# Performance work log

Measured on AMD Instinct MI355X. Metric: run time of the kernel, lower is better.

## Reference

```python
import jax, jax.numpy as jnp
import numpy as np

NUM_Q_HEADS = 32
NUM_KV_HEADS = 8
HEAD_DIM = 128
HIDDEN = 4096
EPS = 1e-6
ROPE_THETA = 1e6


def _rmsnorm(t, w):
    # per-head RMSNorm over last dim (head_dim), as in skip_rmsnorm with residual=None
    var = jnp.mean(t * t, axis=-1, keepdims=True)
    return t * jax.lax.rsqrt(var + EPS) * w


def _rotate_half(t):
    h = t.shape[-1] // 2
    return jnp.concatenate([-t[..., h:], t[..., :h]], axis=-1)


def setup_inputs() -> dict:
    key = jax.random.key(0)
    ks = jax.random.split(key, 4)
    B, S = 2, 1024
    x = jax.random.normal(ks[0], (B, S, HIDDEN), jnp.float32)
    q_proj_w = jax.random.normal(ks[1], (HIDDEN, NUM_Q_HEADS * HEAD_DIM), jnp.float32) * 0.02
    kv_proj_w = jax.random.normal(ks[2], (HIDDEN, 2 * NUM_KV_HEADS * HEAD_DIM), jnp.float32) * 0.02
    o_proj_w = jax.random.normal(ks[3], (NUM_Q_HEADS * HEAD_DIM, HIDDEN), jnp.float32) * 0.02
    q_norm_w = jnp.ones((HEAD_DIM,), jnp.float32)
    k_norm_w = jnp.ones((HEAD_DIM,), jnp.float32)
    # real rotate-half RoPE tables, shape [S, head_dim]
    inv_freq = 1.0 / (ROPE_THETA ** (jnp.arange(0, HEAD_DIM, 2, dtype=jnp.float32) / HEAD_DIM))
    freqs = jnp.arange(S, dtype=jnp.float32)[:, None] * inv_freq[None, :]  # [S, hd/2]
    emb = jnp.concatenate([freqs, freqs], axis=-1)  # [S, hd]
    cos, sin = jnp.cos(emb), jnp.sin(emb)
    kv_buffer = jnp.zeros((16384, 2 * NUM_KV_HEADS, HEAD_DIM), jnp.float32)
    cur_select_index = jnp.arange(B * S, dtype=jnp.int32)
    return {"x": x, "q_proj_w": q_proj_w, "kv_proj_w": kv_proj_w, "o_proj_w": o_proj_w,
            "q_norm_w": q_norm_w, "k_norm_w": k_norm_w, "cos": cos, "sin": sin,
            "kv_buffer": kv_buffer, "cur_select_index": cur_select_index}


def reference(x, q_proj_w, kv_proj_w, o_proj_w, q_norm_w, k_norm_w, cos, sin, kv_buffer, cur_select_index):
    B, S, _ = x.shape
    T = B * S
    xf = x.reshape(T, HIDDEN)
    # projections (weights stored as [in, out])
    xq = (xf @ q_proj_w).reshape(T, NUM_Q_HEADS, HEAD_DIM)
    xkv = xf @ kv_proj_w
    xk = xkv[:, : NUM_KV_HEADS * HEAD_DIM].reshape(T, NUM_KV_HEADS, HEAD_DIM)
    xv = xkv[:, NUM_KV_HEADS * HEAD_DIM:].reshape(T, NUM_KV_HEADS, HEAD_DIM)
    # per-head RMSNorm (Qwen3 q/k norm)
    xq = _rmsnorm(xq, q_norm_w)
    xk = _rmsnorm(xk, k_norm_w)
    # RoPE (cos/sin are [S, hd], tiled over batch, broadcast over heads)
    cos_t = jnp.tile(cos, (B, 1))[:, None, :]  # [T,1,hd]
    sin_t = jnp.tile(sin, (B, 1))[:, None, :]
    xq = xq * cos_t + _rotate_half(xq) * sin_t
    xk = xk * cos_t + _rotate_half(xk) * sin_t
    # paged KV-cache scatter update (update_kv_buffer)
    combined_kv = jnp.concatenate([xk, xv], axis=1)  # [T, 2*Hk, hd]
    buf = kv_buffer.at[cur_select_index].set(combined_kv)
    # ragged causal flash attention (equal per-request lengths here), GQA expand
    rep = NUM_Q_HEADS // NUM_KV_HEADS
    q = xq.reshape(B, S, NUM_Q_HEADS, HEAD_DIM)
    k = jnp.repeat(xk.reshape(B, S, NUM_KV_HEADS, HEAD_DIM), rep, axis=2)
    v = jnp.repeat(xv.reshape(B, S, NUM_KV_HEADS, HEAD_DIM), rep, axis=2)
    scale = HEAD_DIM ** -0.5
    scores = jnp.einsum('bqhd,bkhd->bhqk', q, k) * scale  # [B,H,S,S]
    causal = jnp.tril(jnp.ones((S, S), bool))
    scores = jnp.where(causal[None, None], scores, jnp.float32(-1e30))
    p = jax.nn.softmax(scores, axis=-1)
    attn = jnp.einsum('bhqk,bkhd->bqhd', p, v).reshape(B, S, NUM_Q_HEADS * HEAD_DIM)
    out = attn @ o_proj_w  # [B,S,hidden]
    return out, buf
```

## Files before the change

### kernel.cpp

```cpp
#include <hip/hip_runtime.h>

typedef float fx4 __attribute__((ext_vector_type(4)));
typedef short s16x4 __attribute__((ext_vector_type(4)));
typedef short s16x8 __attribute__((ext_vector_type(8)));
typedef __bf16 bf16x8 __attribute__((ext_vector_type(8)));

__device__ __forceinline__ short f2bf(float f) {
  unsigned u = __builtin_bit_cast(unsigned, f);
  u += 0x7fffu + ((u >> 16) & 1u);
  return (short)(u >> 16);
}
__device__ __forceinline__ float b2f(short s) {
  unsigned u = ((unsigned)(unsigned short)s) << 16;
  return __builtin_bit_cast(float, u);
}

__device__ __forceinline__ bf16x8 ld8(const short* p) {
  s16x8 v = *(const s16x8*)p;
  return __builtin_bit_cast(bf16x8, v);
}

__device__ __forceinline__ void gld16(const void* g, void* l) {
  __builtin_amdgcn_global_load_lds(
      (const __attribute__((address_space(1))) unsigned*)g,
      (__attribute__((address_space(3))) unsigned*)l, 16, 0, 0);
}

template<int N> __device__ __forceinline__ void wait_vmcnt() {
  if constexpr (N == 0)      asm volatile("s_waitcnt vmcnt(0)" ::: "memory");
  else if constexpr (N == 4) asm volatile("s_waitcnt vmcnt(4)" ::: "memory");
  else if constexpr (N == 6) asm volatile("s_waitcnt vmcnt(6)" ::: "memory");
  __builtin_amdgcn_sched_barrier(0);
}

__device__ __forceinline__ void barrier_pin() {
  __builtin_amdgcn_s_barrier();
  __builtin_amdgcn_sched_barrier(0);
}

__global__ __launch_bounds__(256) void cvt_k(const float* __restrict__ in,
                                             short* __restrict__ out) {
  int i = (blockIdx.x * 256 + threadIdx.x) * 8;
  fx4 a = *(const fx4*)(in + i);
  fx4 b = *(const fx4*)(in + i + 4);
  s16x8 w;
  w[0] = f2bf(a[0]); w[1] = f2bf(a[1]); w[2] = f2bf(a[2]); w[3] = f2bf(a[3]);
  w[4] = f2bf(b[0]); w[5] = f2bf(b[1]); w[6] = f2bf(b[2]); w[7] = f2bf(b[3]);
  *(s16x8*)(out + i) = w;
}

__global__ __launch_bounds__(256) void tr_k(const float* __restrict__ in,
    short* __restrict__ out, int K, int N) {
  __shared__ short T[64][72];
  const int ktiles = K >> 6;
  const int tk0 = (blockIdx.x % ktiles) << 6;
  const int tn0 = (blockIdx.x / ktiles) << 6;
  const int tid = threadIdx.x;
  #pragma unroll
  for (int i = 0; i < 4; ++i) {
    int idx = i * 256 + tid;
    int k = idx >> 4, n4 = (idx & 15) << 2;
    fx4 v = *(const fx4*)(in + (size_t)(tk0 + k) * N + tn0 + n4);
    #pragma unroll
    for (int j = 0; j < 4; ++j) T[n4 + j][k] = f2bf(v[j]);
  }
  __syncthreads();
  #pragma unroll
  for (int i = 0; i < 2; ++i) {
    int idx = i * 256 + tid;
    int n = idx >> 3, k8 = (idx & 7) << 3;
    *(s16x8*)(out + (size_t)(tn0 + n) * K + tk0 + k8) = *(const s16x8*)&T[n][k8];
  }
}

__global__ __launch_bounds__(256) void vtr_k(const short* __restrict__ vbp,
                                             short* __restrict__ vbt) {
  __shared__ short T[64][72];
  const int tile = blockIdx.x & 31;
  const int tt = tile & 15, dt = tile >> 4;
  const int bk = blockIdx.x >> 5;
  const int b = bk >> 3, kvh = bk & 7;
  const int t0 = tt << 6, d0 = dt << 6;
  const int tid = threadIdx.x;
  #pragma unroll
  for (int i = 0; i < 2; ++i) {
    int idx = i * 256 + tid;
    int r = idx >> 3, c8 = (idx & 7) << 3;
    s16x8 v = *(const s16x8*)(vbp + (size_t)(b * 1024 + t0 + r) * 1024 + kvh * 128 + d0 + c8);
    #pragma unroll
    for (int j = 0; j < 8; ++j) T[c8 + j][r] = v[j];
  }
  __syncthreads();
  #pragma unroll
  for (int i = 0; i < 2; ++i) {
    int idx = i * 256 + tid;
    int r = idx >> 3, c8 = (idx & 7) << 3;
    *(s16x8*)(vbt + ((size_t)(b * 8 + kvh) * 128 + d0 + r) * 1024 + t0 + c8) =
        *(const s16x8*)&T[r][c8];
  }
}

template<int BF16OUT>
__global__ __launch_bounds__(512) void gemm8(const short* __restrict__ A,
    const short* __restrict__ Bt, void* __restrict__ Cp, int N, int K,
    const fx4* __restrict__ csrc, fx4* __restrict__ cdst, int gemmBlocks,
    size_t nvec) {
  const int tid = threadIdx.x;
  if ((int)blockIdx.x >= gemmBlocks) {
    size_t stride = (size_t)(gridDim.x - gemmBlocks) * 512;
    for (size_t i = (size_t)((int)blockIdx.x - gemmBlocks) * 512 + tid;
         i < nvec; i += stride)
      cdst[i] = csrc[i];
    return;
  }
  __shared__ short As[2][2][128 * 64];
  __shared__ short Bs[2][2][128 * 64];
  const int tiles_n = N >> 8;
  const int tm = blockIdx.x / tiles_n, tn = blockIdx.x % tiles_n;
  const int lane = tid & 63, wv = tid >> 6;
  const int wm = (wv >> 2) << 6;
  const int wn = (wv & 3) << 5;
  const int r0 = tm << 8, c0 = tn << 8;
  const int lrow = lane & 15, lg = lane >> 4;

  auto stageA = [&](int t, int hh) {
    int k0 = t << 6, s = t & 1;
    #pragma unroll
    for (int i = 0; i < 2; ++i) {
      int c = i * 512 + tid;
      int row = c >> 3, ch = c & 7;
      gld16(A + (size_t)(r0 + hh * 128 + row) * K + k0 + ((ch ^ (row & 7)) << 3),
            &As[s][hh][(i * 512 + wv * 64) * 8]);
    }
  };
  auto stageB = [&](int t, int hh) {
    int k0 = t << 6, s = t & 1;
    #pragma unroll
    for (int i = 0; i < 2; ++i) {
      int c = i * 512 + tid;
      int row = c >> 3, ch = c & 7;
      gld16(Bt + (size_t)(c0 + hh * 128 + row) * K + k0 + ((ch ^ (row & 7)) << 3),
            &Bs[s][hh][(i * 512 + wv * 64) * 8]);
    }
  };

  fx4 acc[2][2][4][2] = {};
  bf16x8 a[4][2], b[2][2];

  auto ldA = [&](int s, int hh) {
    #pragma unroll
    for (int mf = 0; mf < 4; ++mf) {
      int lr = wm + mf * 16 + lrow;
      #pragma unroll
      for (int ks = 0; ks < 2; ++ks)
        a[mf][ks] = ld8(&As[s][hh][lr * 64 + ((((ks << 2) + lg) ^ (lr & 7)) << 3)]);
    }
  };
  auto ldB = [&](int s, int hh) {
    #pragma unroll
    for (int nf = 0; nf < 2; ++nf) {
      int lr = wn + nf * 16 + lrow;
      #pragma unroll
      for (int ks = 0; ks < 2; ++ks)
        b[nf][ks] = ld8(&Bs[s][hh][lr * 64 + ((((ks << 2) + lg) ^ (lr & 7)) << 3)]);
    }
  };

  const int nt = K >> 6;
  stageA(0, 0); stageA(0, 1); stageB(0, 0); stageB(0, 1);
  stageA(1, 0); stageB(1, 1);

  for (int t = 0; t < nt; ++t) {
    const int s = t & 1;
    if (t + 1 < nt) wait_vmcnt<4>(); else wait_vmcnt<0>();
    barrier_pin();
    ldA(s, 0); ldB(s, 0);
    if (t + 1 < nt) stageA(t + 1, 1);
    __builtin_amdgcn_s_setprio(1);
    #pragma unroll
    for (int ks = 0; ks < 2; ++ks)
      #pragma unroll
      for (int mf = 0; mf < 4; ++mf)
        #pragma unroll
        for (int nf = 0; nf < 2; ++nf)
          acc[0][0][mf][nf] = __builtin_amdgcn_mfma_f32_16x16x32_bf16(
              a[mf][ks], b[nf][ks], acc[0][0][mf][nf], 0, 0, 0);
    __builtin_amdgcn_s_setprio(0);
    barrier_pin();
    ldB(s, 1);
    if (t + 1 < nt) stageB(t + 1, 0);
    __builtin_amdgcn_s_setprio(1);
    #pragma unroll
    for (int ks = 0; ks < 2; ++ks)
      #pragma unroll
      for (int mf = 0; mf < 4; ++mf)
        #pragma unroll
        for (int nf = 0; nf < 2; ++nf)
          acc[0][1][mf][nf] = __builtin_amdgcn_mfma_f32_16x16x32_bf16(
              a[mf][ks], b[nf][ks], acc[0][1][mf][nf], 0, 0, 0);
    __builtin_amdgcn_s_setprio(0);
    barrier_pin();
    ldA(s, 1);
    if (t + 2 < nt) stageA(t + 2, 0);
    __builtin_amdgcn_s_setprio(1);
    #pragma unroll
    for (int ks = 0; ks < 2; ++ks)
      #pragma unroll
      for (int mf = 0; mf < 4; ++mf)
        #pragma unroll
        for (int nf = 0; nf < 2; ++nf)
          acc[1][1][mf][nf] = __builtin_amdgcn_mfma_f32_16x16x32_bf16(
              a[mf][ks], b[nf][ks], acc[1][1][mf][nf], 0, 0, 0);
    __builtin_amdgcn_s_setprio(0);
    barrier_pin();
    ldB(s, 0);
    if (t + 2 < nt) stageB(t + 2, 1);
    __builtin_amdgcn_s_setprio(1);
    #pragma unroll
    for (int ks = 0; ks < 2; ++ks)
      #pragma unroll
      for (int mf = 0; mf < 4; ++mf)
        #pragma unroll
        for (int nf = 0; nf < 2; ++nf)
          acc[1][0][mf][nf] = __builtin_amdgcn_mfma_f32_16x16x32_bf16(
              a[mf][ks], b[nf][ks], acc[1][0][mf][nf], 0, 0, 0);
    __builtin_amdgcn_s_setprio(0);
    barrier_pin();
  }
  const int g4 = lg << 2;
  #pragma unroll
  for (int mq = 0; mq < 2; ++mq)
    #pragma unroll
    for (int nq = 0; nq < 2; ++nq)
      #pragma unroll
      for (int mf = 0; mf < 4; ++mf)
        #pragma unroll
        for (int nf = 0; nf < 2; ++nf)
          #pragma unroll
          for (int j = 0; j < 4; ++j) {
            int row = r0 + mq * 128 + wm + mf * 16 + g4 + j;
            int col = c0 + nq * 128 + wn + nf * 16 + lrow;
            if (BF16OUT)
              ((short*)Cp)[(size_t)row * N + col] = f2bf(acc[mq][nq][mf][nf][j]);
            else
              ((float*)Cp)[(size_t)row * N + col] = acc[mq][nq][mf][nf][j];
          }
}

__global__ __launch_bounds__(512) void gemm4(const short* __restrict__ A,
    const short* __restrict__ Bt, float* __restrict__ Cp, int N, int K) {
  __shared__ short As[3][2][128 * 64];
  __shared__ short Bs[3][128 * 64];
  const int tiles_n = N >> 7;
  const int tm = blockIdx.x / tiles_n, tn = blockIdx.x % tiles_n;
  const int tid = threadIdx.x;
  const int lane = tid & 63, wv = tid >> 6;
  const int wm = (wv >> 2) << 6;
  const int wn = (wv & 3) << 5;
  const int r0 = tm << 8, c0 = tn << 7;
  const int lrow = lane & 15, lg = lane >> 4;

  auto stageA = [&](int t, int hh) {
    int k0 = t << 6, s = t % 3;
    #pragma unroll
    for (int i = 0; i < 2; ++i) {
      int c = i * 512 + tid;
      int row = c >> 3, ch = c & 7;
      gld16(A + (size_t)(r0 + hh * 128 + row) * K + k0 + ((ch ^ (row & 7)) << 3),
            &As[s][hh][(i * 512 + wv * 64) * 8]);
    }
  };
  auto stageB = [&](int t) {
    int k0 = t << 6, s = t % 3;
    #pragma unroll
    for (int i = 0; i < 2; ++i) {
      int c = i * 512 + tid;
      int row = c >> 3, ch = c & 7;
      gld16(Bt + (size_t)(c0 + row) * K + k0 + ((ch ^ (row & 7)) << 3),
            &Bs[s][(i * 512 + wv * 64) * 8]);
    }
  };

  fx4 acc[2][4][2] = {};
  bf16x8 a[4][2], b[2][2];

  auto ldA = [&](int s, int hh) {
    #pragma unroll
    for (int mf = 0; mf < 4; ++mf) {
      int lr = wm + mf * 16 + lrow;
      #pragma unroll
      for (int ks = 0; ks < 2; ++ks)
        a[mf][ks] = ld8(&As[s][hh][lr * 64 + ((((ks << 2) + lg) ^ (lr & 7)) << 3)]);
    }
  };
  auto ldB = [&](int s) {
    #pragma unroll
    for (int nf = 0; nf < 2; ++nf) {
      int lr = wn + nf * 16 + lrow;
      #pragma unroll
      for (int ks = 0; ks < 2; ++ks)
        b[nf][ks] = ld8(&Bs[s][lr * 64 + ((((ks << 2) + lg) ^ (lr & 7)) << 3)]);
    }
  };

  const int nt = K >> 6;
  stageA(0, 0); stageA(0, 1); stageB(0);
  stageA(1, 0); stageA(1, 1); stageB(1);

  for (int t = 0; t < nt; ++t) {
    const int s = t % 3;
    if (t + 1 < nt) wait_vmcnt<6>(); else wait_vmcnt<0>();
    barrier_pin();
    ldA(s, 0); ldB(s);
    if (t + 2 < nt) stageA(t + 2, 0);
    __builtin_amdgcn_s_setprio(1);
    #pragma unroll
    for (int ks = 0; ks < 2; ++ks)
      #pragma unroll
      for (int mf = 0; mf < 4; ++mf)
        #pragma unroll
        for (int nf = 0; nf < 2; ++nf)
          acc[0][mf][nf] = __builtin_amdgcn_mfma_f32_16x16x32_bf16(
              a[mf][ks], b[nf][ks], acc[0][mf][nf], 0, 0, 0);
    __builtin_amdgcn_s_setprio(0);
    barrier_pin();
    ldA(s, 1);
    if (t + 2 < nt) { stageA(t + 2, 1); stageB(t + 2); }
    __builtin_amdgcn_s_setprio(1);
    #pragma unroll
    for (int ks = 0; ks < 2; ++ks)
      #pragma unroll
      for (int mf = 0; mf < 4; ++mf)
        #pragma unroll
        for (int nf = 0; nf < 2; ++nf)
          acc[1][mf][nf] = __builtin_amdgcn_mfma_f32_16x16x32_bf16(
              a[mf][ks], b[nf][ks], acc[1][mf][nf], 0, 0, 0);
    __builtin_amdgcn_s_setprio(0);
    barrier_pin();
  }
  const int g4 = lg << 2;
  #pragma unroll
  for (int mh = 0; mh < 2; ++mh)
    #pragma unroll
    for (int mf = 0; mf < 4; ++mf)
      #pragma unroll
      for (int nf = 0; nf < 2; ++nf)
        #pragma unroll
        for (int j = 0; j < 4; ++j) {
          int row = r0 + mh * 128 + wm + mf * 16 + g4 + j;
          int col = c0 + wn + nf * 16 + lrow;
          Cp[(size_t)row * N + col] = acc[mh][mf][nf][j];
        }
}

__global__ __launch_bounds__(256) void nr_k(const short* __restrict__ xqkv,
    const float* __restrict__ qnw, const float* __restrict__ knw,
    const float* __restrict__ cosb, const float* __restrict__ sinb,
    const int* __restrict__ idx,
    short* __restrict__ qb, short* __restrict__ kbp, short* __restrict__ vbp,
    float* __restrict__ bufo) {
  int rid = blockIdx.x * 4 + (threadIdx.x >> 6);
  int l = threadIdx.x & 63;
  int type, t, h;
  if (rid < 65536)      { type = 0; t = rid >> 5; h = rid & 31; }
  else if (rid < 81920) { type = 1; int r = rid - 65536; t = r >> 3; h = r & 7; }
  else                  { type = 2; int r = rid - 81920; t = r >> 3; h = r & 7; }
  int s = t & 1023;
  const short* src = xqkv + (size_t)t * 6144 +
                     ((type == 0) ? h * 128 : (type == 1) ? 4096 + h * 128
                                                          : 5120 + h * 128);
  float e0 = b2f(src[l]), e1 = b2f(src[l + 64]);
  float out0, out1;
  if (type < 2) {
    float ss = e0 * e0 + e1 * e1;
    #pragma unroll
    for (int off = 1; off < 64; off <<= 1) ss += __shfl_xor(ss, off);
    float r = rsqrtf(ss * (1.0f / 128.0f) + 1e-6f);
    const float* nw = (type == 0) ? qnw : knw;
    float n0 = e0 * r * nw[l], n1 = e1 * r * nw[l + 64];
    float c0 = cosb[s * 128 + l], c1 = cosb[s * 128 + 64 + l];
    float s0 = sinb[s * 128 + l], s1 = sinb[s * 128 + 64 + l];
    out0 = n0 * c0 - n1 * s0;
    out1 = n1 * c1 + n0 * s1;
  } else { out0 = e0; out1 = e1; }
  if (type == 0) {
    short* d = qb + (size_t)t * 4096 + h * 128;
    d[l] = f2bf(out0); d[l + 64] = f2bf(out1);
  } else {
    int br = idx[t];
    float* bd = bufo + (size_t)br * 2048 + (type == 1 ? 0 : 1024) + h * 128;
    bd[l] = out0; bd[l + 64] = out1;
    short* d = (type == 1) ? kbp + (size_t)t * 1024 + h * 128
                           : vbp + (size_t)t * 1024 + h * 128;
    d[l] = f2bf(out0); d[l + 64] = f2bf(out1);
  }
}

#define KLD 136
#define PLD 72

__global__ __launch_bounds__(512) void attn_k(const short* __restrict__ qb,
    const short* __restrict__ kbp, const short* __restrict__ vbt,
    short* __restrict__ ob) {
  __shared__ short Ks[64 * KLD];
  __shared__ short Vs[128 * 64];
  __shared__ short Ps[8][16 * PLD];
  const int bid = blockIdx.x;
  const int p = 7 - (bid & 7), h = (bid >> 3) & 31, b = bid >> 8;
  const int kvh = h >> 2;
  const int tid = threadIdx.x, lane = tid & 63, w = tid >> 6;
  const int lrow = lane & 15, lg = lane >> 4, lk = lg << 3;
  const int q0 = p << 7;
  const int ktmax = 2 * p + 1;
  const float SC2 = 0.088388347648318447f * 1.4426950408889634f;

  bf16x8 qf[4];
  {
    const short* qp = qb + ((size_t)(b * 1024 + q0 + w * 16 + lrow) * 32 + h) * 128 + lk;
    #pragma unroll
    for (int kb4 = 0; kb4 < 4; ++kb4) qf[kb4] = ld8(qp + kb4 * 32);
  }

  const short* vt_base = vbt + (size_t)(b * 8 + kvh) * 128 * 1024;

  const int sd8 = (tid & 15) << 3;
  s16x8 kreg[2], vreg[2];
  auto ldkv = [&](int kv0) {
    #pragma unroll
    for (int it = 0; it < 2; ++it) {
      int r = (it << 5) + (tid >> 4);
      kreg[it] = *(const s16x8*)(kbp + ((size_t)(b * 1024 + kv0 + r) * 8 + kvh) * 128 + sd8);
      int d = (it << 6) + (tid >> 3);
      vreg[it] = *(const s16x8*)(vt_base + (size_t)d * 1024 + kv0 + ((tid & 7) << 3));
    }
  };
  auto wrkv = [&]() {
    #pragma unroll
    for (int it = 0; it < 2; ++it) {
      int r = (it << 5) + (tid >> 4);
      *(s16x8*)&Ks[r * KLD + sd8] = kreg[it];
      int d = (it << 6) + (tid >> 3);
      *(s16x8*)&Vs[d * 64 + (((tid & 7) ^ (d & 7)) << 3)] = vreg[it];
    }
  };

  float m[4], lsum[4];
  fx4 acc[8] = {};
  #pragma unroll
  for (int j = 0; j < 4; ++j) { m[j] = -3.0e38f; lsum[j] = 0.f; }

  ldkv(0);
  wrkv();
  __syncthreads();

  for (int kt = 0; kt <= ktmax; ++kt) {
    const int kv0 = kt << 6;
    if (kt < ktmax) ldkv((kt + 1) << 6);
    fx4 sf[4];
    #pragma unroll
    for (int nc = 0; nc < 4; ++nc) {
      fx4 z = {0.f, 0.f, 0.f, 0.f};
      sf[nc] = z;
      #pragma unroll
      for (int kb4 = 0; kb4 < 4; ++kb4) {
        bf16x8 kf = ld8(&Ks[(nc * 16 + lrow) * KLD + kb4 * 32 + lk]);
        sf[nc] = __builtin_amdgcn_mfma_f32_16x16x32_bf16(qf[kb4], kf, sf[nc], 0, 0, 0);
      }
    }
    if (kt >= ktmax - 1) {
      #pragma unroll
      for (int nc = 0; nc < 4; ++nc)
        #pragma unroll
        for (int j = 0; j < 4; ++j) {
          int qr = q0 + w * 16 + (lg << 2) + j;
          int kc = kv0 + nc * 16 + lrow;
          if (kc > qr) sf[nc][j] = -3.0e38f;
        }
    }
    float pm[4];
    #pragma unroll
    for (int j = 0; j < 4; ++j) pm[j] = -3.0e38f;
    #pragma unroll
    for (int nc = 0; nc < 4; ++nc)
      #pragma unroll
      for (int j = 0; j < 4; ++j) pm[j] = fmaxf(pm[j], sf[nc][j]);
    #pragma unroll
    for (int j = 0; j < 4; ++j) {
      pm[j] = fmaxf(pm[j], __shfl_xor(pm[j], 1));
      pm[j] = fmaxf(pm[j], __shfl_xor(pm[j], 2));
      pm[j] = fmaxf(pm[j], __shfl_xor(pm[j], 4));
      pm[j] = fmaxf(pm[j], __shfl_xor(pm[j], 8));
    }
    float alpha[4], rs[4];
    #pragma unroll
    for (int j = 0; j < 4; ++j) {
      float mn = fmaxf(m[j], pm[j]);
      alpha[j] = exp2f((m[j] - mn) * SC2);
      m[j] = mn;
      rs[j] = 0.f;
    }
    #pragma unroll
    for (int nc = 0; nc < 4; ++nc)
      #pragma unroll
      for (int j = 0; j < 4; ++j) {
        float pv = exp2f((sf[nc][j] - m[j]) * SC2);
        rs[j] += pv;
        Ps[w][((lg << 2) + j) * PLD + nc * 16 + lrow] = f2bf(pv);
      }
    #pragma unroll
    for (int j = 0; j < 4; ++j) {
      rs[j] += __shfl_xor(rs[j], 1);
      rs[j] += __shfl_xor(rs[j], 2);
      rs[j] += __shfl_xor(rs[j], 4);
      rs[j] += __shfl_xor(rs[j], 8);
      lsum[j] = lsum[j] * alpha[j] + rs[j];
    }
    #pragma unroll
    for (int dg = 0; dg < 8; ++dg)
      #pragma unroll
      for (int j = 0; j < 4; ++j) acc[dg][j] *= alpha[j];
    #pragma unroll
    for (int kb2 = 0; kb2 < 2; ++kb2) {
      bf16x8 pf = ld8(&Ps[w][lrow * PLD + kb2 * 32 + lk]);
      #pragma unroll
      for (int dg = 0; dg < 8; ++dg) {
        int d = dg * 16 + lrow;
        int tch = (kb2 << 2) + lg;
        bf16x8 vf = ld8(&Vs[d * 64 + ((tch ^ (d & 7)) << 3)]);
        acc[dg] = __builtin_amdgcn_mfma_f32_16x16x32_bf16(pf, vf, acc[dg], 0, 0, 0);
      }
    }
    __syncthreads();
    if (kt < ktmax) {
      wrkv();
      __syncthreads();
    }
  }
  #pragma unroll
  for (int j = 0; j < 4; ++j) {
    float rl = 1.0f / lsum[j];
    int t = b * 1024 + q0 + w * 16 + (lg << 2) + j;
    short* op = ob + ((size_t)t * 32 + h) * 128;
    #pragma unroll
    for (int dg = 0; dg < 8; ++dg)
      op[dg * 16 + lrow] = f2bf(acc[dg][j] * rl);
  }
}

extern "C" void kernel_launch(void* const* d_in, const int* in_sizes, int n_in,
                              void* d_out, int out_size, void* d_ws, size_t ws_size,
                              hipStream_t stream) {
  (void)in_sizes; (void)n_in; (void)out_size; (void)ws_size;
  const float* x    = (const float*)d_in[0];
  const float* qw   = (const float*)d_in[1];
  const float* kvw  = (const float*)d_in[2];
  const float* ow   = (const float*)d_in[3];
  const float* qnw  = (const float*)d_in[4];
  const float* knw  = (const float*)d_in[5];
  const float* cosb = (const float*)d_in[6];
  const float* sinb = (const float*)d_in[7];
  const float* kvbf = (const float*)d_in[8];
  const int*   idx  = (const int*)d_in[9];

  float* outp = (float*)d_out;
  float* bufp = outp + (size_t)2048 * 4096;

  char* ws = (char*)d_ws;
  short* xqkv = (short*)ws;
  short* qb   = (short*)(ws + (size_t)2048 * 6144 * 4);
  short* kbp  = (short*)((char*)qb + (size_t)2048 * 4096 * 2);
  short* vbp  = (short*)((char*)kbp + (size_t)2048 * 1024 * 2);
  short* attnb = (short*)(ws + (size_t)2048 * 6144 * 2);
  short* owt   = (short*)((char*)qb + (size_t)2048 * 4096 * 2 + (size_t)2048 * 2048 * 2 * 2);
  short* vbt   = owt;

  short* xb    = (short*)bufp;
  short* wqkvt = (short*)(bufp + (size_t)2048 * 2048);

  cvt_k<<<dim3(4096), dim3(256), 0, stream>>>(x, xb);
  tr_k<<<dim3(64 * 64), dim3(256), 0, stream>>>(qw, wqkvt, 4096, 4096);
  tr_k<<<dim3(64 * 32), dim3(256), 0, stream>>>(kvw, wqkvt + (size_t)4096 * 4096, 4096, 2048);
  {
    const fx4* csrc = (const fx4*)(kvbf + (size_t)8192 * 2048);
    fx4* cdst = (fx4*)(bufp + (size_t)8192 * 2048);
    size_t nvec = (size_t)8192 * 2048 / 4;
    gemm8<1><<<dim3(256), dim3(512), 0, stream>>>(xb, wqkvt, (void*)xqkv, 6144, 4096,
                                                  csrc, cdst, 192, nvec);
  }
  hipMemcpyAsync(bufp + (size_t)2048 * 2048, kvbf + (size_t)2048 * 2048,
                 (size_t)6144 * 2048 * 4, hipMemcpyDeviceToDevice, stream);
  nr_k<<<dim3(98304 / 4), dim3(256), 0, stream>>>(xqkv, qnw, knw, cosb, sinb, idx,
                                                  qb, kbp, vbp, bufp);
  vtr_k<<<dim3(512), dim3(256), 0, stream>>>(vbp, vbt);
  attn_k<<<dim3(2 * 32 * 8), dim3(512), 0, stream>>>(qb, kbp, vbt, attnb);
  tr_k<<<dim3(64 * 64), dim3(256), 0, stream>>>(ow, owt, 4096, 4096);
  gemm4<<<dim3(8 * 32), dim3(512), 0, stream>>>(attnb, owt, outp, 4096, 4096);
}
```

Baseline: 364.1 us.

## Split-K the output GEMM with 256x256 tiles and fold the KV copy into attention

The output projection GEMM now uses 256x256 tiles with a 2-way split-K. Chunk 0 writes fp32 directly, chunk 1 writes bf16 partials, and a small reduction kernel adds them. The tail copy of the KV buffer moves from a hipMemcpyAsync into 64 extra blocks of the attention kernel, so it overlaps with attention compute. The bf16 partial adds rounding error, and the split-K costs an extra reduction pass plus extra memory traffic.

```diff
diff --git a/kernel.cpp b/kernel.cpp
--- a/kernel.cpp
+++ b/kernel.cpp
@@ -247,21 +247,24 @@
           }
 }
 
-__global__ __launch_bounds__(512) void gemm4(const short* __restrict__ A,
-    const short* __restrict__ Bt, float* __restrict__ Cp, int N, int K) {
-  __shared__ short As[3][2][128 * 64];
-  __shared__ short Bs[3][128 * 64];
-  const int tiles_n = N >> 7;
-  const int tm = blockIdx.x / tiles_n, tn = blockIdx.x % tiles_n;
+__global__ __launch_bounds__(512) void gemm8sk(const short* __restrict__ A,
+    const short* __restrict__ Bt, float* __restrict__ Cp,
+    short* __restrict__ pK, int N, int K) {
+  __shared__ short As[2][2][128 * 64];
+  __shared__ short Bs[2][2][128 * 64];
+  const int tiles_n = N >> 8;
+  const int tile = blockIdx.x & 127, chunk = blockIdx.x >> 7;
+  const int tm = tile / tiles_n, tn = tile % tiles_n;
+  const int kOff = chunk << 11;
   const int tid = threadIdx.x;
   const int lane = tid & 63, wv = tid >> 6;
   const int wm = (wv >> 2) << 6;
   const int wn = (wv & 3) << 5;
-  const int r0 = tm << 8, c0 = tn << 7;
+  const int r0 = tm << 8, c0 = tn << 8;
   const int lrow = lane & 15, lg = lane >> 4;
 
   auto stageA = [&](int t, int hh) {
-    int k0 = t << 6, s = t % 3;
+    int k0 = kOff + (t << 6), s = t & 1;
     #pragma unroll
     for (int i = 0; i < 2; ++i) {
       int c = i * 512 + tid;
@@ -270,18 +273,18 @@
             &As[s][hh][(i * 512 + wv * 64) * 8]);
     }
   };
-  auto stageB = [&](int t) {
-    int k0 = t << 6, s = t % 3;
+  auto stageB = [&](int t, int hh) {
+    int k0 = kOff + (t << 6), s = t & 1;
     #pragma unroll
     for (int i = 0; i < 2; ++i) {
       int c = i * 512 + tid;
       int row = c >> 3, ch = c & 7;
-      gld16(Bt + (size_t)(c0 + row) * K + k0 + ((ch ^ (row & 7)) << 3),
-            &Bs[s][(i * 512 + wv * 64) * 8]);
-    }
-  };
-
-  fx4 acc[2][4][2] = {};
+      gld16(Bt + (size_t)(c0 + hh * 128 + row) * K + k0 + ((ch ^ (row & 7)) << 3),
+            &Bs[s][hh][(i * 512 + wv * 64) * 8]);
+    }
+  };
+
+  fx4 acc[2][2][4][2] = {};
   bf16x8 a[4][2], b[2][2];
 
   auto ldA = [&](int s, int hh) {
@@ -293,25 +296,51 @@
         a[mf][ks] = ld8(&As[s][hh][lr * 64 + ((((ks << 2) + lg) ^ (lr & 7)) << 3)]);
     }
   };
-  auto ldB = [&](int s) {
+  auto ldB = [&](int s, int hh) {
     #pragma unroll
     for (int nf = 0; nf < 2; ++nf) {
       int lr = wn + nf * 16 + lrow;
       #pragma unroll
       for (int ks = 0; ks < 2; ++ks)
-        b[nf][ks] = ld8(&Bs[s][lr * 64 + ((((ks << 2) + lg) ^ (lr & 7)) << 3)]);
-    }
-  };
-
-  const int nt = K >> 6;
-  stageA(0, 0); stageA(0, 1); stageB(0);
-  stageA(1, 0); stageA(1, 1); stageB(1);
+        b[nf][ks] = ld8(&Bs[s][hh][lr * 64 + ((((ks << 2) + lg) ^ (lr & 7)) << 3)]);
+    }
+  };
+
+  const int nt = 32;
+  stageA(0, 0); stageA(0, 1); stageB(0, 0); stageB(0, 1);
+  stageA(1, 0); stageB(1, 1);
 
   for (int t = 0; t < nt; ++t) {
-    const int s = t % 3;
-    if (t + 1 < nt) wait_vmcnt<6>(); else wait_vmcnt<0>();
-    barrier_pin();
-    ldA(s, 0); ldB(s);
+    const int s = t & 1;
+    if (t + 1 < nt) wait_vmcnt<4>(); else wait_vmcnt<0>();
+    barrier_pin();
+    ldA(s, 0); ldB(s, 0);
+    if (t + 1 < nt) stageA(t + 1, 1);
+    __builtin_amdgcn_s_setprio(1);
+    #pragma unroll
+    for (int ks = 0; ks < 2; ++ks)
+      #pragma unroll
+      for (int mf = 0; mf < 4; ++mf)
+        #pragma unroll
+        for (int nf = 0; nf < 2; ++nf)
+          acc[0][0][mf][nf] = __builtin_amdgcn_mfma_f32_16x16x32_bf16(
+              a[mf][ks], b[nf][ks], acc[0][0][mf][nf], 0, 0, 0);
+    __builtin_amdgcn_s_setprio(0);
+    barrier_pin();
+    ldB(s, 1);
+    if (t + 1 < nt) stageB(t + 1, 0);
+    __builtin_amdgcn_s_setprio(1);
+    #pragma unroll
+    for (int ks = 0; ks < 2; ++ks)
+      #pragma unroll
+      for (int mf = 0; mf < 4; ++mf)
+        #pragma unroll
+        for (int nf = 0; nf < 2; ++nf)
+          acc[0][1][mf][nf] = __builtin_amdgcn_mfma_f32_16x16x32_bf16(
+              a[mf][ks], b[nf][ks], acc[0][1][mf][nf], 0, 0, 0);
+    __builtin_amdgcn_s_setprio(0);
+    barrier_pin();
+    ldA(s, 1);
     if (t + 2 < nt) stageA(t + 2, 0);
     __builtin_amdgcn_s_setprio(1);
     #pragma unroll
@@ -320,37 +349,51 @@
       for (int mf = 0; mf < 4; ++mf)
         #pragma unroll
         for (int nf = 0; nf < 2; ++nf)
-          acc[0][mf][nf] = __builtin_amdgcn_mfma_f32_16x16x32_bf16(
-              a[mf][ks], b[nf][ks], acc[0][mf][nf], 0, 0, 0);
-    __builtin_amdgcn_s_setprio(0);
-    barrier_pin();
-    ldA(s, 1);
-    if (t + 2 < nt) { stageA(t + 2, 1); stageB(t + 2); }
-    __builtin_amdgcn_s_setprio(1);
-    #pragma unroll
-    for (int ks = 0; ks < 2; ++ks)
-      #pragma unroll
-      for (int mf = 0; mf < 4; ++mf)
-        #pragma unroll
-        for (int nf = 0; nf < 2; ++nf)
-          acc[1][mf][nf] = __builtin_amdgcn_mfma_f32_16x16x32_bf16(
-              a[mf][ks], b[nf][ks], acc[1][mf][nf], 0, 0, 0);
+          acc[1][1][mf][nf] = __builtin_amdgcn_mfma_f32_16x16x32_bf16(
+              a[mf][ks], b[nf][ks], acc[1][1][mf][nf], 0, 0, 0);
+    __builtin_amdgcn_s_setprio(0);
+    barrier_pin();
+    ldB(s, 0);
+    if (t + 2 < nt) stageB(t + 2, 1);
+    __builtin_amdgcn_s_setprio(1);
+    #pragma unroll
+    for (int ks = 0; ks < 2; ++ks)
+      #pragma unroll
+      for (int mf = 0; mf < 4; ++mf)
+        #pragma unroll
+        for (int nf = 0; nf < 2; ++nf)
+          acc[1][0][mf][nf] = __builtin_amdgcn_mfma_f32_16x16x32_bf16(
+              a[mf][ks], b[nf][ks], acc[1][0][mf][nf], 0, 0, 0);
     __builtin_amdgcn_s_setprio(0);
     barrier_pin();
   }
   const int g4 = lg << 2;
   #pragma unroll
-  for (int mh = 0; mh < 2; ++mh)
-    #pragma unroll
-    for (int mf = 0; mf < 4; ++mf)
-      #pragma unroll
-      for (int nf = 0; nf < 2; ++nf)
-        #pragma unroll
-        for (int j = 0; j < 4; ++j) {
-          int row = r0 + mh * 128 + wm + mf * 16 + g4 + j;
-          int col = c0 + wn + nf * 16 + lrow;
-          Cp[(size_t)row * N + col] = acc[mh][mf][nf][j];
-        }
+  for (int mq = 0; mq < 2; ++mq)
+    #pragma unroll
+    for (int nq = 0; nq < 2; ++nq)
+      #pragma unroll
+      for (int mf = 0; mf < 4; ++mf)
+        #pragma unroll
+        for (int nf = 0; nf < 2; ++nf)
+          #pragma unroll
+          for (int j = 0; j < 4; ++j) {
+            int row = r0 + mq * 128 + wm + mf * 16 + g4 + j;
+            int col = c0 + nq * 128 + wn + nf * 16 + lrow;
+            if (chunk == 0)
+              Cp[(size_t)row * N + col] = acc[mq][nq][mf][nf][j];
+            else
+              pK[(size_t)row * N + col] = f2bf(acc[mq][nq][mf][nf][j]);
+          }
+}
+
+__global__ __launch_bounds__(256) void red_k(float* __restrict__ outp,
+                                             const short* __restrict__ pK) {
+  size_t i = ((size_t)blockIdx.x * 256 + threadIdx.x) * 4;
+  fx4 o = *(fx4*)(outp + i);
+  s16x4 p = *(const s16x4*)(pK + i);
+  o[0] += b2f(p[0]); o[1] += b2f(p[1]); o[2] += b2f(p[2]); o[3] += b2f(p[3]);
+  *(fx4*)(outp + i) = o;
 }
 
 __global__ __launch_bounds__(256) void nr_k(const short* __restrict__ xqkv,
@@ -398,17 +441,26 @@
 
 #define KLD 136
 #define PLD 72
+#define CPB 64
 
 __global__ __launch_bounds__(512) void attn_k(const short* __restrict__ qb,
     const short* __restrict__ kbp, const short* __restrict__ vbt,
-    short* __restrict__ ob) {
+    short* __restrict__ ob, const fx4* __restrict__ csrc,
+    fx4* __restrict__ cdst, size_t nvec) {
   __shared__ short Ks[64 * KLD];
   __shared__ short Vs[128 * 64];
   __shared__ short Ps[8][16 * PLD];
-  const int bid = blockIdx.x;
+  const int tid = threadIdx.x;
+  if ((int)blockIdx.x < CPB) {
+    size_t stride = (size_t)CPB * 512;
+    for (size_t i = (size_t)blockIdx.x * 512 + tid; i < nvec; i += stride)
+      cdst[i] = csrc[i];
+    return;
+  }
+  const int bid = blockIdx.x - CPB;
   const int p = 7 - (bid & 7), h = (bid >> 3) & 31, b = bid >> 8;
   const int kvh = h >> 2;
-  const int tid = threadIdx.x, lane = tid & 63, w = tid >> 6;
+  const int lane = tid & 63, w = tid >> 6;
   const int lrow = lane & 15, lg = lane >> 4, lk = lg << 3;
   const int q0 = p << 7;
   const int ktmax = 2 * p + 1;
@@ -573,6 +625,7 @@
   short* attnb = (short*)(ws + (size_t)2048 * 6144 * 2);
   short* owt   = (short*)((char*)qb + (size_t)2048 * 4096 * 2 + (size_t)2048 * 2048 * 2 * 2);
   short* vbt   = owt;
+  short* pK    = xqkv;
 
   short* xb    = (short*)bufp;
   short* wqkvt = (short*)(bufp + (size_t)2048 * 2048);
@@ -587,12 +640,17 @@
     gemm8<1><<<dim3(256), dim3(512), 0, stream>>>(xb, wqkvt, (void*)xqkv, 6144, 4096,
                                                   csrc, cdst, 192, nvec);
   }
-  hipMemcpyAsync(bufp + (size_t)2048 * 2048, kvbf + (size_t)2048 * 2048,
-                 (size_t)6144 * 2048 * 4, hipMemcpyDeviceToDevice, stream);
   nr_k<<<dim3(98304 / 4), dim3(256), 0, stream>>>(xqkv, qnw, knw, cosb, sinb, idx,
                                                   qb, kbp, vbp, bufp);
   vtr_k<<<dim3(512), dim3(256), 0, stream>>>(vbp, vbt);
-  attn_k<<<dim3(2 * 32 * 8), dim3(512), 0, stream>>>(qb, kbp, vbt, attnb);
+  {
+    const fx4* csrc = (const fx4*)(kvbf + (size_t)2048 * 2048);
+    fx4* cdst = (fx4*)(bufp + (size_t)2048 * 2048);
+    size_t nvec = (size_t)6144 * 2048 / 4;
+    attn_k<<<dim3(2 * 32 * 8 + CPB), dim3(512), 0, stream>>>(qb, kbp, vbt, attnb,
+                                                             csrc, cdst, nvec);
+  }
   tr_k<<<dim3(64 * 64), dim3(256), 0, stream>>>(ow, owt, 4096, 4096);
-  gemm4<<<dim3(8 * 32), dim3(512), 0, stream>>>(attnb, owt, outp, 4096, 4096);
-}
+  gemm8sk<<<dim3(256), dim3(512), 0, stream>>>(attnb, owt, outp, pK, 4096, 4096);
+  red_k<<<dim3(8192), dim3(256), 0, stream>>>(outp, pK);
+}
```

After: 396.6 us. 1.09x slower.

## Merge prologue kernels and overlap o_proj weight transpose with attention

Applied to the files above, without the earlier changes.

Folds the x conversion and both QKV weight transposes into one prologue launch. The o_proj weight transpose moves into 64 extra blocks of the attention kernel so it runs alongside attention instead of as a separate kernel. The KV-buffer copy moves to the end of the stream, and owt now reuses the bufp scratch region that the copy later overwrites. This removes launch gaps and tail idle time, at the cost of tying up 64 CUs with transpose work during attention and depending on the copy ordering for correctness of the buffer region.

```diff
diff --git a/kernel.cpp b/kernel.cpp
--- a/kernel.cpp
+++ b/kernel.cpp
@@ -38,24 +38,27 @@
   __builtin_amdgcn_sched_barrier(0);
 }
 
-__global__ __launch_bounds__(256) void cvt_k(const float* __restrict__ in,
-                                             short* __restrict__ out) {
-  int i = (blockIdx.x * 256 + threadIdx.x) * 8;
-  fx4 a = *(const fx4*)(in + i);
-  fx4 b = *(const fx4*)(in + i + 4);
-  s16x8 w;
-  w[0] = f2bf(a[0]); w[1] = f2bf(a[1]); w[2] = f2bf(a[2]); w[3] = f2bf(a[3]);
-  w[4] = f2bf(b[0]); w[5] = f2bf(b[1]); w[6] = f2bf(b[2]); w[7] = f2bf(b[3]);
-  *(s16x8*)(out + i) = w;
-}
-
-__global__ __launch_bounds__(256) void tr_k(const float* __restrict__ in,
-    short* __restrict__ out, int K, int N) {
+__global__ __launch_bounds__(256) void pro_k(const float* __restrict__ x,
+    short* __restrict__ xb, const float* __restrict__ qw,
+    const float* __restrict__ kvw, short* __restrict__ wqkvt) {
   __shared__ short T[64][72];
-  const int ktiles = K >> 6;
-  const int tk0 = (blockIdx.x % ktiles) << 6;
-  const int tn0 = (blockIdx.x / ktiles) << 6;
   const int tid = threadIdx.x;
+  const int blk = blockIdx.x;
+  if (blk < 4096) {
+    int i = (blk * 256 + tid) * 8;
+    fx4 a = *(const fx4*)(x + i);
+    fx4 b = *(const fx4*)(x + i + 4);
+    s16x8 w;
+    w[0] = f2bf(a[0]); w[1] = f2bf(a[1]); w[2] = f2bf(a[2]); w[3] = f2bf(a[3]);
+    w[4] = f2bf(b[0]); w[5] = f2bf(b[1]); w[6] = f2bf(b[2]); w[7] = f2bf(b[3]);
+    *(s16x8*)(xb + i) = w;
+    return;
+  }
+  const float* in; short* out; int N, t;
+  if (blk < 8192) { in = qw;  out = wqkvt;                          N = 4096; t = blk - 4096; }
+  else            { in = kvw; out = wqkvt + (size_t)4096 * 4096;    N = 2048; t = blk - 8192; }
+  const int tk0 = (t & 63) << 6;
+  const int tn0 = (t >> 6) << 6;
   #pragma unroll
   for (int i = 0; i < 4; ++i) {
     int idx = i * 256 + tid;
@@ -69,7 +72,7 @@
   for (int i = 0; i < 2; ++i) {
     int idx = i * 256 + tid;
     int n = idx >> 3, k8 = (idx & 7) << 3;
-    *(s16x8*)(out + (size_t)(tn0 + n) * K + tk0 + k8) = *(const s16x8*)&T[n][k8];
+    *(s16x8*)(out + (size_t)(tn0 + n) * 4096 + tk0 + k8) = *(const s16x8*)&T[n][k8];
   }
 }
 
@@ -398,17 +401,42 @@
 
 #define KLD 136
 #define PLD 72
+#define TRB 64
 
 __global__ __launch_bounds__(512) void attn_k(const short* __restrict__ qb,
     const short* __restrict__ kbp, const short* __restrict__ vbt,
-    short* __restrict__ ob) {
+    short* __restrict__ ob, const float* __restrict__ ow,
+    short* __restrict__ owt) {
   __shared__ short Ks[64 * KLD];
   __shared__ short Vs[128 * 64];
   __shared__ short Ps[8][16 * PLD];
-  const int bid = blockIdx.x;
+  const int tid = threadIdx.x;
+  if ((int)blockIdx.x < TRB) {
+    short (*T)[72] = (short(*)[72])Ks;
+    for (int t = (int)blockIdx.x; t < 4096; t += TRB) {
+      const int tk0 = (t & 63) << 6;
+      const int tn0 = (t >> 6) << 6;
+      #pragma unroll
+      for (int i = 0; i < 2; ++i) {
+        int idx = i * 512 + tid;
+        int k = idx >> 4, n4 = (idx & 15) << 2;
+        fx4 v = *(const fx4*)(ow + (size_t)(tk0 + k) * 4096 + tn0 + n4);
+        #pragma unroll
+        for (int j = 0; j < 4; ++j) T[n4 + j][k] = f2bf(v[j]);
+      }
+      __syncthreads();
+      {
+        int n = tid >> 3, k8 = (tid & 7) << 3;
+        *(s16x8*)(owt + (size_t)(tn0 + n) * 4096 + tk0 + k8) = *(const s16x8*)&T[n][k8];
+      }
+      __syncthreads();
+    }
+    return;
+  }
+  const int bid = blockIdx.x - TRB;
   const int p = 7 - (bid & 7), h = (bid >> 3) & 31, b = bid >> 8;
   const int kvh = h >> 2;
-  const int tid = threadIdx.x, lane = tid & 63, w = tid >> 6;
+  const int lane = tid & 63, w = tid >> 6;
   const int lrow = lane & 15, lg = lane >> 4, lk = lg << 3;
   const int q0 = p << 7;
   const int ktmax = 2 * p + 1;
@@ -567,19 +595,17 @@
 
   char* ws = (char*)d_ws;
   short* xqkv = (short*)ws;
+  short* attnb = (short*)(ws + (size_t)2048 * 6144 * 2);
   short* qb   = (short*)(ws + (size_t)2048 * 6144 * 4);
   short* kbp  = (short*)((char*)qb + (size_t)2048 * 4096 * 2);
   short* vbp  = (short*)((char*)kbp + (size_t)2048 * 1024 * 2);
-  short* attnb = (short*)(ws + (size_t)2048 * 6144 * 2);
-  short* owt   = (short*)((char*)qb + (size_t)2048 * 4096 * 2 + (size_t)2048 * 2048 * 2 * 2);
-  short* vbt   = owt;
+  short* vbt  = (short*)((char*)vbp + (size_t)2048 * 1024 * 2);
 
   short* xb    = (short*)bufp;
   short* wqkvt = (short*)(bufp + (size_t)2048 * 2048);
-
-  cvt_k<<<dim3(4096), dim3(256), 0, stream>>>(x, xb);
-  tr_k<<<dim3(64 * 64), dim3(256), 0, stream>>>(qw, wqkvt, 4096, 4096);
-  tr_k<<<dim3(64 * 32), dim3(256), 0, stream>>>(kvw, wqkvt + (size_t)4096 * 4096, 4096, 2048);
+  short* owt   = (short*)(bufp + (size_t)2048 * 2048);
+
+  pro_k<<<dim3(10240), dim3(256), 0, stream>>>(x, xb, qw, kvw, wqkvt);
   {
     const fx4* csrc = (const fx4*)(kvbf + (size_t)8192 * 2048);
     fx4* cdst = (fx4*)(bufp + (size_t)8192 * 2048);
@@ -587,12 +613,11 @@
     gemm8<1><<<dim3(256), dim3(512), 0, stream>>>(xb, wqkvt, (void*)xqkv, 6144, 4096,
                                                   csrc, cdst, 192, nvec);
   }
-  hipMemcpyAsync(bufp + (size_t)2048 * 2048, kvbf + (size_t)2048 * 2048,
-                 (size_t)6144 * 2048 * 4, hipMemcpyDeviceToDevice, stream);
   nr_k<<<dim3(98304 / 4), dim3(256), 0, stream>>>(xqkv, qnw, knw, cosb, sinb, idx,
                                                   qb, kbp, vbp, bufp);
   vtr_k<<<dim3(512), dim3(256), 0, stream>>>(vbp, vbt);
-  attn_k<<<dim3(2 * 32 * 8), dim3(512), 0, stream>>>(qb, kbp, vbt, attnb);
-  tr_k<<<dim3(64 * 64), dim3(256), 0, stream>>>(ow, owt, 4096, 4096);
+  attn_k<<<dim3(2 * 32 * 8 + TRB), dim3(512), 0, stream>>>(qb, kbp, vbt, attnb, ow, owt);
   gemm4<<<dim3(8 * 32), dim3(512), 0, stream>>>(attnb, owt, outp, 4096, 4096);
-}
+  hipMemcpyAsync(bufp + (size_t)2048 * 2048, kvbf + (size_t)2048 * 2048,
+                 (size_t)6144 * 2048 * 4, hipMemcpyDeviceToDevice, stream);
+}
```

Result: no change. 370.0 us (+1.6%).
